# Optimization experiments

Measured on AMD Instinct MI355X. Metric: run time of the kernel, lower is better.

The kernel has to match this reference:

```python
import jax, jax.numpy as jnp
import numpy as np

N_G, N_D, D = 50000, 50000, 64
R, L, NNZ, B = 32, 2, 1600000, 2048
TEMP, LAMBDA_1, LAMBDA_2, DROPOUT = 0.2, 0.2, 1e-7, 0.1


def setup_inputs() -> dict:
    key = jax.random.key(0)
    ks = jax.random.split(key, 14)
    uids = jax.random.randint(ks[0], (B,), 0, N_G)
    iids = jax.random.randint(ks[1], (B,), 0, N_D)
    pos = jax.random.randint(ks[2], (B,), 0, N_D)
    neg = jax.random.randint(ks[3], (B,), 0, N_D)
    E_g_0 = jax.random.normal(ks[4], (N_G, D), jnp.float32) * 0.01
    E_d_0 = jax.random.normal(ks[5], (N_D, D), jnp.float32) * 0.01
    rows = jax.random.randint(ks[6], (NNZ,), 0, N_G)
    cols = jax.random.randint(ks[7], (NNZ,), 0, N_D)
    vals = jax.random.uniform(ks[8], (NNZ,), jnp.float32)
    g_mul_s = jax.random.normal(ks[9], (N_G, R), jnp.float32) * 0.1
    v_mul_s = jax.random.normal(ks[10], (N_D, R), jnp.float32) * 0.1
    ut = jax.random.normal(ks[11], (R, N_G), jnp.float32) * (N_G ** -0.5)
    vt = jax.random.normal(ks[12], (R, N_D), jnp.float32) * (N_D ** -0.5)
    drop_u = jax.random.uniform(ks[13], (L, 2, NNZ), jnp.float32)
    return {"uids": uids, "iids": iids, "pos": pos, "neg": neg,
            "E_g_0": E_g_0, "E_d_0": E_d_0, "rows": rows, "cols": cols,
            "vals": vals, "g_mul_s": g_mul_s, "v_mul_s": v_mul_s,
            "ut": ut, "vt": vt, "drop_u": drop_u}


def reference(uids, iids, pos, neg, E_g_0, E_d_0, rows, cols, vals,
              g_mul_s, v_mul_s, ut, vt, drop_u):
    # sparse_dropout keep masks (independent per layer and per spmm call)
    keep = (drop_u > DROPOUT).astype(vals.dtype) / (1.0 - DROPOUT)  # [L,2,NNZ]
    E_g, E_d = E_g_0, E_d_0
    E_g_sum, E_d_sum = E_g_0, E_d_0
    G_g_sum, G_d_sum = E_g_0, E_d_0
    for layer in range(L):
        # Z_g = dropout(A) @ E_d ; Z_d = dropout(A).T @ E_g  (COO spmm)
        vg = vals * keep[layer, 0]
        Z_g = jax.ops.segment_sum(vg[:, None] * E_d[cols], rows, num_segments=N_G)
        vd = vals * keep[layer, 1]
        Z_d = jax.ops.segment_sum(vd[:, None] * E_g[rows], cols, num_segments=N_D)
        # low-rank SVD branch
        G_g = g_mul_s @ (vt @ E_d)  # [n_g, d]
        G_d = v_mul_s @ (ut @ E_g)  # [n_d, d]
        E_g, E_d = Z_g, Z_d
        E_g_sum = E_g_sum + E_g
        E_d_sum = E_d_sum + E_d
        G_g_sum = G_g_sum + G_g
        G_d_sum = G_d_sum + G_d
    # InfoNCE-style contrastive loss (exactly as torch: log(sum exp + eps))
    S_g = (G_g_sum[uids] @ E_g_sum.T) / TEMP  # [B, n_g]
    S_d = (G_d_sum[iids] @ E_d_sum.T) / TEMP  # [B, n_d]
    neg_score = jnp.log(jnp.exp(S_g).sum(1) + 1e-8).mean() \
              + jnp.log(jnp.exp(S_d).sum(1) + 1e-8).mean()
    pos_score = jnp.clip((G_g_sum[uids] * E_g_sum[uids]).sum(1) / TEMP, -5.0, 5.0).mean() \
              + jnp.clip((G_d_sum[iids] * E_d_sum[iids]).sum(1) / TEMP, -5.0, 5.0).mean()
    loss_s = -pos_score + neg_score
    # BPR loss
    g_emb = E_g_sum[uids]
    diff = (g_emb * E_d_sum[pos]).sum(-1) - (g_emb * E_d_sum[neg]).sum(-1)
    loss_r = -jnp.log(jax.nn.sigmoid(diff)).mean()
    # L2 reg over trainable embedding params
    loss_reg = LAMBDA_2 * (jnp.sum(E_g_0 ** 2) + jnp.sum(E_d_0 ** 2))
    loss = loss_r + LAMBDA_1 * loss_s + loss_reg
    return (loss, loss_r, LAMBDA_1 * loss_s)
```

## Files before the change

kernel.cpp:

```cpp
#include <hip/hip_runtime.h>
#include <hip/hip_bf16.h>
#include <math.h>

#define N_Gc 50000
#define N_Dc 50000
#define DIM 64
#define RNK 32
#define NNZc 1600000
#define BSZ 2048
#define KEEPV (1.0f/0.9f)
#define INVT 5.0f
#define NBK2 196
#define NBLK 200
#define NSL 24
#define EPB 8000
#define MCH 256
#define MBLK 196

typedef __attribute__((ext_vector_type(8))) short bfrag;
typedef __attribute__((ext_vector_type(4))) float f32x4;

__device__ inline ushort f2bf(float f) {
  union { float f; unsigned int u; } v; v.f = f;
  unsigned int r = (v.u + 0x7fffu + ((v.u >> 16) & 1u)) >> 16;
  return (ushort)r;
}
__device__ inline float bf2f(ushort u) {
  union { unsigned int i; float f; } v; v.i = ((unsigned int)u) << 16;
  return v.f;
}

__global__ __launch_bounds__(256) void hist3_kernel(const int* __restrict__ rows, const int* __restrict__ cols,
                                                    int* __restrict__ cntR, int* __restrict__ cntC) {
  __shared__ int lh_r[NBK2];
  __shared__ int lh_c[NBK2];
  int t = threadIdx.x, blk = blockIdx.x;
  if (t < NBK2) { lh_r[t] = 0; lh_c[t] = 0; }
  __syncthreads();
  int e0 = blk*EPB;
  for (int i = e0 + t; i < e0 + EPB; i += 256) {
    atomicAdd(&lh_r[rows[i] >> 8], 1);
    atomicAdd(&lh_c[cols[i] >> 8], 1);
  }
  __syncthreads();
  if (t < NBK2) {
    cntR[t*NBLK + blk] = lh_r[t];
    cntC[t*NBLK + blk] = lh_c[t];
  }
}

__global__ __launch_bounds__(1024) void cscan2_kernel(const int* __restrict__ cntA, int* __restrict__ cbA, int* __restrict__ bpA,
                                                      const int* __restrict__ cntB, int* __restrict__ cbB, int* __restrict__ bpB) {
  const int n = NBK2*NBLK;
  const int* cnt = blockIdx.x ? cntB : cntA;
  int* cb = blockIdx.x ? cbB : cbA;
  int* bp = blockIdx.x ? bpB : bpA;
  __shared__ int wsum[16];
  int t = threadIdx.x, lane = t & 63, w = t >> 6;
  int carry = 0;
  for (int base = 0; base < n; base += 1024) {
    int i = base + t;
    int v = (i < n) ? cnt[i] : 0;
    int x = v;
    #pragma unroll
    for (int o = 1; o < 64; o <<= 1) { int y = __shfl_up(x, o); if (lane >= o) x += y; }
    if (lane == 63) wsum[w] = x;
    __syncthreads();
    if (t < 16) {
      int s = wsum[t];
      #pragma unroll
      for (int o = 1; o < 16; o <<= 1) { int y = __shfl_up(s, o); if (t >= o) s += y; }
      wsum[t] = s;
    }
    __syncthreads();
    int wpre = (w == 0) ? 0 : wsum[w-1];
    int total = wsum[15];
    int ex = carry + wpre + (x - v);
    if (i < n) {
      cb[i] = ex;
      if (i % NBLK == 0) bp[i/NBLK] = ex;
    }
    carry += total;
    __syncthreads();
  }
  if (t == 0) bp[NBK2] = carry;
}

__global__ __launch_bounds__(256) void phaseA2_kernel(const int* __restrict__ rows, const int* __restrict__ cols,
    const float* __restrict__ vals, const float* __restrict__ drop,
    const int* __restrict__ cbR, const int* __restrict__ cbC,
    uint2* __restrict__ stage_r, uint2* __restrict__ stage_c) {
  __shared__ int cnt_r[NBK2], cnt_c[NBK2];
  __shared__ int base_r[NBK2], base_c[NBK2];
  int t = threadIdx.x, blk = blockIdx.x;
  if (t < NBK2) {
    cnt_r[t] = 0; cnt_c[t] = 0;
    base_r[t] = cbR[t*NBLK + blk];
    base_c[t] = cbC[t*NBLK + blk];
  }
  __syncthreads();
  int e0 = blk*EPB;
  for (int i = e0 + t; i < e0 + EPB; i += 256) {
    int r = rows[i], c = cols[i];
    unsigned int vb = __float_as_uint(vals[i]);
    unsigned int dr0 = (drop[i] > 0.1f) ? (1u<<24) : 0u;
    unsigned int dc0 = (drop[(size_t)NNZc + i] > 0.1f) ? (1u<<24) : 0u;
    unsigned int dr1 = (drop[2*(size_t)NNZc + i] > 0.1f) ? (1u<<25) : 0u;
    unsigned int dc1 = (drop[3*(size_t)NNZc + i] > 0.1f) ? (1u<<25) : 0u;
    int br = r >> 8, bc = c >> 8;
    int p = base_r[br] + atomicAdd(&cnt_r[br], 1);
    stage_r[p] = make_uint2((unsigned int)c | ((unsigned int)(r & 255) << 16) | dr0 | dr1, vb);
    int q = base_c[bc] + atomicAdd(&cnt_c[bc], 1);
    stage_c[q] = make_uint2((unsigned int)r | ((unsigned int)(c & 255) << 16) | dc0 | dc1, vb);
  }
}

__global__ __launch_bounds__(256) void phaseB2_kernel(const int* __restrict__ bptr, int* __restrict__ ptrout,
    const uint2* __restrict__ stage, ushort* __restrict__ fcol,
    float* __restrict__ fw0, float* __restrict__ fw1, int n) {
  __shared__ int cnt[256];
  __shared__ int pos[256];
  __shared__ int woff[4];
  int t = threadIdx.x, b = blockIdx.x;
  int base_row = b*256;
  int base = bptr[b], endp = bptr[b+1];
  cnt[t] = 0;
  __syncthreads();
  for (int k = base + t; k < endp; k += 256)
    atomicAdd(&cnt[(stage[k].x >> 16) & 255], 1);
  __syncthreads();
  int lane = t & 63, w = t >> 6;
  int c = cnt[t], x = c;
  #pragma unroll
  for (int o = 1; o < 64; o <<= 1) { int y = __shfl_up(x, o); if (lane >= o) x += y; }
  if (lane == 63) woff[w] = x;
  __syncthreads();
  if (t == 0) { woff[1] += woff[0]; woff[2] += woff[1]; woff[3] += woff[2]; }
  __syncthreads();
  int excl = ((w == 0) ? 0 : woff[w-1]) + (x - c);
  pos[t] = excl;
  int rr = base_row + t;
  if (rr <= n) ptrout[rr] = base + excl;
  __syncthreads();
  for (int k = base + t; k < endp; k += 256) {
    uint2 rec = stage[k];
    int rel = (rec.x >> 16) & 255;
    int p = base + atomicAdd(&pos[rel], 1);
    float v = __uint_as_float(rec.y);
    fcol[p] = (ushort)(rec.x & 0xffffu);
    fw0[p] = (rec.x & (1u<<24)) ? v*KEEPV : 0.f;
    fw1[p] = (rec.x & (1u<<25)) ? v*KEEPV : 0.f;
  }
}

__global__ __launch_bounds__(256) void spmm_l0_kernel(const int* __restrict__ ptr,
    const ushort* __restrict__ fcol, const float* __restrict__ fw,
    const ushort* __restrict__ Eb, float* __restrict__ Z, ushort* __restrict__ Zb, int nrows) {
  int lane = threadIdx.x & 63;
  int row = blockIdx.x*4 + (threadIdx.x >> 6);
  if (row >= nrows) return;
  int k = ptr[row], end = ptr[row+1];
  float acc = 0.f;
  for (; k + 8 <= end; k += 8) {
    int cc[8]; float ww[8]; float gg[8];
    #pragma unroll
    for (int u = 0; u < 8; u++) { cc[u] = fcol[k+u]; ww[u] = fw[k+u]; }
    #pragma unroll
    for (int u = 0; u < 8; u++) gg[u] = bf2f(Eb[(size_t)cc[u]*DIM + lane]);
    #pragma unroll
    for (int u = 0; u < 8; u++) acc += ww[u]*gg[u];
  }
  for (; k < end; k++)
    acc += fw[k]*bf2f(Eb[(size_t)fcol[k]*DIM + lane]);
  size_t o = (size_t)row*DIM + lane;
  Z[o] = acc;
  Zb[o] = f2bf(acc);
}

__global__ __launch_bounds__(256) void spmm_l1_kernel(const int* __restrict__ ptr,
    const ushort* __restrict__ fcol, const float* __restrict__ fw,
    const ushort* __restrict__ Zb, const float* __restrict__ addA, const float* __restrict__ addB,
    ushort* __restrict__ Eout, int nrows) {
  int lane = threadIdx.x & 63;
  int row = blockIdx.x*4 + (threadIdx.x >> 6);
  if (row >= nrows) return;
  int k = ptr[row], end = ptr[row+1];
  float acc = 0.f;
  for (; k + 8 <= end; k += 8) {
    int cc[8]; float ww[8]; float gg[8];
    #pragma unroll
    for (int u = 0; u < 8; u++) { cc[u] = fcol[k+u]; ww[u] = fw[k+u]; }
    #pragma unroll
    for (int u = 0; u < 8; u++) gg[u] = bf2f(Zb[(size_t)cc[u]*DIM + lane]);
    #pragma unroll
    for (int u = 0; u < 8; u++) acc += ww[u]*gg[u];
  }
  for (; k < end; k++)
    acc += fw[k]*bf2f(Zb[(size_t)fcol[k]*DIM + lane]);
  size_t o = (size_t)row*DIM + lane;
  acc += addA[o] + addB[o];
  Eout[o] = f2bf(acc);
}

__global__ __launch_bounds__(256) void matred2_kernel(const float* __restrict__ vrow,
    const float* __restrict__ E0, const float* __restrict__ Z0,
    float* __restrict__ Mpart, int n) {
  __shared__ float vs[RNK*MCH];
  __shared__ float part[RNK*DIM];
  int t = threadIdx.x, lane = t & 63, w = t >> 6;
  int ci0 = blockIdx.x*MCH;
  int cnt = min(MCH, n - ci0);
  for (int idx = t; idx < RNK*DIM; idx += 256) part[idx] = 0.f;
  for (int idx = t; idx < RNK*MCH; idx += 256) {
    int r = idx >> 8, i = idx & (MCH-1);
    vs[idx] = (i < cnt) ? vrow[(size_t)r*n + ci0 + i] : 0.f;
  }
  __syncthreads();
  float acc[RNK];
  #pragma unroll
  for (int r = 0; r < RNK; r++) acc[r] = 0.f;
  int iw0 = w*64;
  for (int ii = 0; ii < 64; ii += 4) {
    int i = iw0 + ii;
    int gi = ci0 + i;
    float x0 = 0.f, x1 = 0.f, x2 = 0.f, x3 = 0.f;
    if (i + 3 < cnt) {
      x0 = E0[(size_t)(gi+0)*DIM + lane] + Z0[(size_t)(gi+0)*DIM + lane];
      x1 = E0[(size_t)(gi+1)*DIM + lane] + Z0[(size_t)(gi+1)*DIM + lane];
      x2 = E0[(size_t)(gi+2)*DIM + lane] + Z0[(size_t)(gi+2)*DIM + lane];
      x3 = E0[(size_t)(gi+3)*DIM + lane] + Z0[(size_t)(gi+3)*DIM + lane];
    } else {
      if (i+0 < cnt) x0 = E0[(size_t)(gi+0)*DIM + lane] + Z0[(size_t)(gi+0)*DIM + lane];
      if (i+1 < cnt) x1 = E0[(size_t)(gi+1)*DIM + lane] + Z0[(size_t)(gi+1)*DIM + lane];
      if (i+2 < cnt) x2 = E0[(size_t)(gi+2)*DIM + lane] + Z0[(size_t)(gi+2)*DIM + lane];
      if (i+3 < cnt) x3 = E0[(size_t)(gi+3)*DIM + lane] + Z0[(size_t)(gi+3)*DIM + lane];
    }
    #pragma unroll
    for (int r = 0; r < RNK; r++) {
      float4 v4 = *(const float4*)&vs[r*MCH + i];
      acc[r] += v4.x*x0 + v4.y*x1 + v4.z*x2 + v4.w*x3;
    }
  }
  #pragma unroll
  for (int r = 0; r < RNK; r++) atomicAdd(&part[r*DIM + lane], acc[r]);
  __syncthreads();
  float* dst = Mpart + (size_t)blockIdx.x*(RNK*DIM);
  for (int idx = t; idx < RNK*DIM; idx += 256) dst[idx] = part[idx];
}

__global__ __launch_bounds__(256) void mreduce_kernel(const float* __restrict__ Mpart,
    float* __restrict__ M, int nblk) {
  int idx = blockIdx.x*256 + threadIdx.x;
  if (idx < RNK*DIM) {
    float s = 0.f;
    for (int b = 0; b < nblk; b++) s += Mpart[(size_t)b*(RNK*DIM) + idx];
    M[idx] = s;
  }
}

__global__ __launch_bounds__(256) void gsmall_kernel(const int* __restrict__ ids,
    const float* __restrict__ E0, const float* __restrict__ mul, const float* __restrict__ M,
    float* __restrict__ out, ushort* __restrict__ outb) {
  __shared__ float Ms[RNK*DIM];
  int t = threadIdx.x;
  for (int i = t; i < RNK*DIM; i += 256) Ms[i] = M[i];
  __syncthreads();
  int b = blockIdx.x*4 + (t >> 6), lane = t & 63;
  int u = ids[b];
  float a = E0[(size_t)u*DIM + lane];
  #pragma unroll
  for (int r = 0; r < RNK; r++) a += mul[(size_t)u*RNK + r]*Ms[r*DIM + lane];
  out[(size_t)b*DIM + lane] = a;
  outb[(size_t)b*DIM + lane] = f2bf(a);
}

__global__ __launch_bounds__(256) void convsq_kernel(const float4* __restrict__ in,
    ushort4* __restrict__ out, int n4, float* __restrict__ acc) {
  __shared__ float ls[4];
  int t = threadIdx.x;
  int idx = blockIdx.x*256 + t;
  int stride = gridDim.x*256;
  float s = 0.f;
  for (int i = idx; i < n4; i += stride) {
    float4 v = in[i];
    ushort4 o;
    o.x = f2bf(v.x); o.y = f2bf(v.y); o.z = f2bf(v.z); o.w = f2bf(v.w);
    out[i] = o;
    s += v.x*v.x + v.y*v.y + v.z*v.z + v.w*v.w;
  }
  #pragma unroll
  for (int o = 32; o > 0; o >>= 1) s += __shfl_xor(s, o);
  if ((t & 63) == 0) ls[t >> 6] = s;
  __syncthreads();
  if (t == 0) atomicAdd(acc, ls[0] + ls[1] + ls[2] + ls[3]);
}

__global__ __launch_bounds__(256) void lse_mfma_kernel(const ushort* __restrict__ A,
    const ushort* __restrict__ X, int nj, float* __restrict__ sumexp) {
  __shared__ __align__(16) ushort Xs[64*68];
  int t = threadIdx.x, lane = t & 63, w = t >> 6;
  int bt = blockIdx.x & 31, js = blockIdx.x >> 5;
  int b0 = bt*64;
  int m = lane & 15, q = lane >> 4;
  const ushort* Arow = A + (size_t)(b0 + w*16 + m)*DIM + q*8;
  bfrag a0 = *(const bfrag*)(Arow);
  bfrag a1 = *(const bfrag*)(Arow + 32);
  float rs0 = 0.f, rs1 = 0.f, rs2 = 0.f, rs3 = 0.f;
  int njt = (nj + 63) >> 6;
  for (int jt = js; jt < njt; jt += NSL) {
    int j0 = jt << 6;
    __syncthreads();
    for (int c = t; c < 512; c += 256) {
      int r = c >> 3, k8 = (c & 7) << 3;
      int j = j0 + r;
      ushort4 v0 = {0,0,0,0}, v1 = {0,0,0,0};
      if (j < nj) {
        const ushort4* src = (const ushort4*)(X + (size_t)j*DIM + k8);
        v0 = src[0]; v1 = src[1];
      }
      *(ushort4*)&Xs[r*68 + k8]     = v0;
      *(ushort4*)&Xs[r*68 + k8 + 4] = v1;
    }
    __syncthreads();
    #pragma unroll
    for (int jq = 0; jq < 4; jq++) {
      int jr = jq*16 + m;
      union { bfrag f; uint2 u2[2]; } B0, B1;
      B0.u2[0] = *(const uint2*)&Xs[jr*68 + q*8];
      B0.u2[1] = *(const uint2*)&Xs[jr*68 + q*8 + 4];
      B1.u2[0] = *(const uint2*)&Xs[jr*68 + 32 + q*8];
      B1.u2[1] = *(const uint2*)&Xs[jr*68 + 32 + q*8 + 4];
      f32x4 acc = {0.f, 0.f, 0.f, 0.f};
      acc = __builtin_amdgcn_mfma_f32_16x16x32_bf16(a0, B0.f, acc, 0, 0, 0);
      acc = __builtin_amdgcn_mfma_f32_16x16x32_bf16(a1, B1.f, acc, 0, 0, 0);
      int jg = j0 + jr;
      if (jg < nj) {
        rs0 += __expf(acc[0]*INVT);
        rs1 += __expf(acc[1]*INVT);
        rs2 += __expf(acc[2]*INVT);
        rs3 += __expf(acc[3]*INVT);
      }
    }
  }
  #pragma unroll
  for (int o = 1; o < 16; o <<= 1) {
    rs0 += __shfl_xor(rs0, o);
    rs1 += __shfl_xor(rs1, o);
    rs2 += __shfl_xor(rs2, o);
    rs3 += __shfl_xor(rs3, o);
  }
  if (m == 0) {
    float* dst = &sumexp[b0 + w*16 + q*4];
    atomicAdd(&dst[0], rs0);
    atomicAdd(&dst[1], rs1);
    atomicAdd(&dst[2], rs2);
    atomicAdd(&dst[3], rs3);
  }
}

__global__ __launch_bounds__(256) void perb_kernel(const int* __restrict__ uids, const int* __restrict__ iids,
    const int* __restrict__ pos, const int* __restrict__ neg,
    const float* __restrict__ Ggu, const float* __restrict__ Gdi,
    const ushort* __restrict__ Egs_b, const ushort* __restrict__ Eds_b,
    const float* __restrict__ seg, const float* __restrict__ sed,
    float* __restrict__ accs) {
  __shared__ float lsum[3][4];
  int t = threadIdx.x, lane = t & 63, w = t >> 6;
  int b = blockIdx.x*4 + w;
  int u = uids[b], it = iids[b], p = pos[b], ng = neg[b];
  float egu = bf2f(Egs_b[(size_t)u*DIM + lane]);
  float d1 = Ggu[(size_t)b*DIM + lane]*egu;
  float d2 = Gdi[(size_t)b*DIM + lane]*bf2f(Eds_b[(size_t)it*DIM + lane]);
  float d3 = egu*bf2f(Eds_b[(size_t)p*DIM + lane]);
  float d4 = egu*bf2f(Eds_b[(size_t)ng*DIM + lane]);
  #pragma unroll
  for (int o = 32; o > 0; o >>= 1) {
    d1 += __shfl_xor(d1, o);
    d2 += __shfl_xor(d2, o);
    d3 += __shfl_xor(d3, o);
    d4 += __shfl_xor(d4, o);
  }
  if (lane == 0) {
    float pterm = fminf(fmaxf(d1*INVT, -5.f), 5.f) + fminf(fmaxf(d2*INVT, -5.f), 5.f);
    float diff = d3 - d4;
    lsum[0][w] = pterm;
    lsum[1][w] = log1pf(expf(-diff));
    lsum[2][w] = logf(seg[b] + 1e-8f) + logf(sed[b] + 1e-8f);
  }
  __syncthreads();
  if (t < 3) atomicAdd(&accs[t], lsum[t][0] + lsum[t][1] + lsum[t][2] + lsum[t][3]);
}

__global__ void final_kernel(const float* __restrict__ accs, float* __restrict__ out) {
  float posm = accs[0]*(1.f/BSZ);
  float lr   = accs[1]*(1.f/BSZ);
  float negm = accs[2]*(1.f/BSZ);
  float reg  = 1e-7f*accs[3];
  float l1ls = 0.2f*(negm - posm);
  out[0] = lr + l1ls + reg;
  out[1] = lr;
  out[2] = l1ls;
}

extern "C" void kernel_launch(void* const* d_in, const int* in_sizes, int n_in,
                              void* d_out, int out_size, void* d_ws, size_t ws_size,
                              hipStream_t stream) {
  (void)in_sizes; (void)n_in; (void)out_size;
  const int*   uids = (const int*)d_in[0];
  const int*   iids = (const int*)d_in[1];
  const int*   pos  = (const int*)d_in[2];
  const int*   neg  = (const int*)d_in[3];
  const float* Eg0  = (const float*)d_in[4];
  const float* Ed0  = (const float*)d_in[5];
  const int*   rows = (const int*)d_in[6];
  const int*   cols = (const int*)d_in[7];
  const float* vals = (const float*)d_in[8];
  const float* gms  = (const float*)d_in[9];
  const float* vms  = (const float*)d_in[10];
  const float* ut   = (const float*)d_in[11];
  const float* vt   = (const float*)d_in[12];
  const float* drop = (const float*)d_in[13];
  float* out = (float*)d_out;

  float* ws = (float*)d_ws;
  const size_t ED = (size_t)N_Gc*DIM;
  float* Zg0  = ws;
  float* Zd0  = Zg0 + ED;
  float* REG1 = Zd0 + ED;
  float* REG2 = REG1 + ED;
  int* ptr_r = (int*)(REG2 + ED);
  int* ptr_c = ptr_r + (N_Gc + 1);
  int* bptr_r = ptr_c + (N_Dc + 1);
  int* bptr_c = bptr_r + (NBK2 + 1);
  int* cntR = bptr_c + (NBK2 + 1);
  int* cntC = cntR + NBK2*NBLK;
  int* cbR  = cntC + NBK2*NBLK;
  int* cbC  = cbR + NBK2*NBLK;
  ushort* fcol_r = (ushort*)(cbC + NBK2*NBLK);
  float* fw_r0  = (float*)(fcol_r + NNZc);
  float* fw_r1  = fw_r0 + NNZc;
  ushort* fcol_c = (ushort*)(fw_r1 + NNZc);
  float* fw_c0  = (float*)(fcol_c + NNZc);
  float* fw_c1  = fw_c0 + NNZc;
  float* Ggu = fw_c1 + NNZc;
  float* Gdi = Ggu + (size_t)BSZ*DIM;
  ushort* Ggu_b = (ushort*)(Gdi + (size_t)BSZ*DIM);
  ushort* Gdi_b = Ggu_b + (size_t)BSZ*DIM;
  float* Mg  = (float*)(Gdi_b + (size_t)BSZ*DIM);
  float* Md  = Mg + RNK*DIM;
  float* seg = Md + RNK*DIM;
  float* sed = seg + BSZ;
  float* accs = sed + BSZ;
  float* MpG = accs + 16;
  float* MpD = MpG + (size_t)MBLK*RNK*DIM;

  uint2* stage_r = (uint2*)Zg0;
  uint2* stage_c = (uint2*)REG1;
  ushort* Eg0_b = (ushort*)REG1;
  ushort* Ed0_b = Eg0_b + ED;
  ushort* Egs_b = (ushort*)REG1;
  ushort* Eds_b = Egs_b + ED;
  ushort* Zg0_b = (ushort*)REG2;
  ushort* Zd0_b = Zg0_b + ED;

  size_t need = ((char*)(MpD + (size_t)MBLK*RNK*DIM)) - ((char*)d_ws);
  if (ws_size < need) return;

  hipMemsetAsync(seg, 0, sizeof(float)*(2*BSZ + 16), stream);

  hist3_kernel<<<NBLK, 256, 0, stream>>>(rows, cols, cntR, cntC);
  cscan2_kernel<<<2, 1024, 0, stream>>>(cntR, cbR, bptr_r, cntC, cbC, bptr_c);
  phaseA2_kernel<<<NBLK, 256, 0, stream>>>(rows, cols, vals, drop, cbR, cbC, stage_r, stage_c);
  phaseB2_kernel<<<NBK2, 256, 0, stream>>>(bptr_r, ptr_r, stage_r, fcol_r, fw_r0, fw_r1, N_Gc);
  phaseB2_kernel<<<NBK2, 256, 0, stream>>>(bptr_c, ptr_c, stage_c, fcol_c, fw_c0, fw_c1, N_Dc);

  int n4 = (int)(ED/4);
  convsq_kernel<<<1024, 256, 0, stream>>>((const float4*)Eg0, (ushort4*)Eg0_b, n4, accs + 3);
  convsq_kernel<<<1024, 256, 0, stream>>>((const float4*)Ed0, (ushort4*)Ed0_b, n4, accs + 3);

  int spmm_blocks = (N_Gc + 3)/4;
  spmm_l0_kernel<<<spmm_blocks, 256, 0, stream>>>(ptr_r, fcol_r, fw_r0, Ed0_b, Zg0, Zg0_b, N_Gc);
  spmm_l0_kernel<<<spmm_blocks, 256, 0, stream>>>(ptr_c, fcol_c, fw_c0, Eg0_b, Zd0, Zd0_b, N_Dc);
  spmm_l1_kernel<<<spmm_blocks, 256, 0, stream>>>(ptr_r, fcol_r, fw_r1, Zd0_b, Eg0, Zg0, Egs_b, N_Gc);
  spmm_l1_kernel<<<spmm_blocks, 256, 0, stream>>>(ptr_c, fcol_c, fw_c1, Zg0_b, Ed0, Zd0, Eds_b, N_Dc);

  matred2_kernel<<<MBLK, 256, 0, stream>>>(vt, Ed0, Zd0, MpG, N_Dc);
  matred2_kernel<<<MBLK, 256, 0, stream>>>(ut, Eg0, Zg0, MpD, N_Gc);
  mreduce_kernel<<<(RNK*DIM + 255)/256, 256, 0, stream>>>(MpG, Mg, MBLK);
  mreduce_kernel<<<(RNK*DIM + 255)/256, 256, 0, stream>>>(MpD, Md, MBLK);

  gsmall_kernel<<<BSZ/4, 256, 0, stream>>>(uids, Eg0, gms, Mg, Ggu, Ggu_b);
  gsmall_kernel<<<BSZ/4, 256, 0, stream>>>(iids, Ed0, vms, Md, Gdi, Gdi_b);

  lse_mfma_kernel<<<32*NSL, 256, 0, stream>>>(Ggu_b, Egs_b, N_Gc, seg);
  lse_mfma_kernel<<<32*NSL, 256, 0, stream>>>(Gdi_b, Eds_b, N_Dc, sed);

  perb_kernel<<<BSZ/4, 256, 0, stream>>>(uids, iids, pos, neg, Ggu, Gdi, Egs_b, Eds_b, seg, sed, accs);
  final_kernel<<<1, 1, 0, stream>>>(accs, out);
}
```

Baseline: 687.2 us.

## Merge paired kernels via blockIdx.y, drop fp32 Z buffers, add nontemporal loads and prefetch

Each pair of row-side and column-side kernel launches (phaseB2, convsq, spmm l0/l1, matred2, mreduce, gsmall, lse) becomes a single launch with a second grid dimension choosing the side. Launch count drops and the two independent halves can run concurrently. The fp32 Z intermediates are removed: later stages read the bf16 copies, which cuts workspace and traffic but adds bf16 rounding to the residual sums. Streaming data now uses nontemporal loads and stores, the spmm index/weight fetch is software-prefetched one chunk ahead, and the LSE slice count is doubled.

```diff
diff --git a/kernel.cpp b/kernel.cpp
--- a/kernel.cpp
+++ b/kernel.cpp
@@ -12,13 +12,14 @@
 #define INVT 5.0f
 #define NBK2 196
 #define NBLK 200
-#define NSL 24
+#define NSL 48
 #define EPB 8000
 #define MCH 256
 #define MBLK 196
 
 typedef __attribute__((ext_vector_type(8))) short bfrag;
 typedef __attribute__((ext_vector_type(4))) float f32x4;
+typedef unsigned long long u64;
 
 __device__ inline ushort f2bf(float f) {
   union { float f; unsigned int u; } v; v.f = f;
@@ -39,8 +40,8 @@
   __syncthreads();
   int e0 = blk*EPB;
   for (int i = e0 + t; i < e0 + EPB; i += 256) {
-    atomicAdd(&lh_r[rows[i] >> 8], 1);
-    atomicAdd(&lh_c[cols[i] >> 8], 1);
+    atomicAdd(&lh_r[__builtin_nontemporal_load(&rows[i]) >> 8], 1);
+    atomicAdd(&lh_c[__builtin_nontemporal_load(&cols[i]) >> 8], 1);
   }
   __syncthreads();
   if (t < NBK2) {
@@ -89,7 +90,7 @@
 __global__ __launch_bounds__(256) void phaseA2_kernel(const int* __restrict__ rows, const int* __restrict__ cols,
     const float* __restrict__ vals, const float* __restrict__ drop,
     const int* __restrict__ cbR, const int* __restrict__ cbC,
-    uint2* __restrict__ stage_r, uint2* __restrict__ stage_c) {
+    u64* __restrict__ stage_r, u64* __restrict__ stage_c) {
   __shared__ int cnt_r[NBK2], cnt_c[NBK2];
   __shared__ int base_r[NBK2], base_c[NBK2];
   int t = threadIdx.x, blk = blockIdx.x;
@@ -101,23 +102,35 @@
   __syncthreads();
   int e0 = blk*EPB;
   for (int i = e0 + t; i < e0 + EPB; i += 256) {
-    int r = rows[i], c = cols[i];
-    unsigned int vb = __float_as_uint(vals[i]);
-    unsigned int dr0 = (drop[i] > 0.1f) ? (1u<<24) : 0u;
-    unsigned int dc0 = (drop[(size_t)NNZc + i] > 0.1f) ? (1u<<24) : 0u;
-    unsigned int dr1 = (drop[2*(size_t)NNZc + i] > 0.1f) ? (1u<<25) : 0u;
-    unsigned int dc1 = (drop[3*(size_t)NNZc + i] > 0.1f) ? (1u<<25) : 0u;
+    int r = __builtin_nontemporal_load(&rows[i]);
+    int c = __builtin_nontemporal_load(&cols[i]);
+    u64 vb = (u64)__float_as_uint(__builtin_nontemporal_load(&vals[i])) << 32;
+    unsigned int dr0 = (__builtin_nontemporal_load(&drop[i]) > 0.1f) ? (1u<<24) : 0u;
+    unsigned int dc0 = (__builtin_nontemporal_load(&drop[(size_t)NNZc + i]) > 0.1f) ? (1u<<24) : 0u;
+    unsigned int dr1 = (__builtin_nontemporal_load(&drop[2*(size_t)NNZc + i]) > 0.1f) ? (1u<<25) : 0u;
+    unsigned int dc1 = (__builtin_nontemporal_load(&drop[3*(size_t)NNZc + i]) > 0.1f) ? (1u<<25) : 0u;
     int br = r >> 8, bc = c >> 8;
     int p = base_r[br] + atomicAdd(&cnt_r[br], 1);
-    stage_r[p] = make_uint2((unsigned int)c | ((unsigned int)(r & 255) << 16) | dr0 | dr1, vb);
+    u64 recr = vb | (unsigned int)c | ((unsigned int)(r & 255) << 16) | dr0 | dr1;
+    __builtin_nontemporal_store(recr, &stage_r[p]);
     int q = base_c[bc] + atomicAdd(&cnt_c[bc], 1);
-    stage_c[q] = make_uint2((unsigned int)r | ((unsigned int)(c & 255) << 16) | dc0 | dc1, vb);
-  }
-}
-
-__global__ __launch_bounds__(256) void phaseB2_kernel(const int* __restrict__ bptr, int* __restrict__ ptrout,
-    const uint2* __restrict__ stage, ushort* __restrict__ fcol,
-    float* __restrict__ fw0, float* __restrict__ fw1, int n) {
+    u64 recc = vb | (unsigned int)r | ((unsigned int)(c & 255) << 16) | dc0 | dc1;
+    __builtin_nontemporal_store(recc, &stage_c[q]);
+  }
+}
+
+__global__ __launch_bounds__(256) void phaseB2_kernel(
+    const int* __restrict__ bptrR, int* __restrict__ ptroutR, const u64* __restrict__ stageR,
+    ushort* __restrict__ fcolR, float* __restrict__ fw0R, float* __restrict__ fw1R,
+    const int* __restrict__ bptrC, int* __restrict__ ptroutC, const u64* __restrict__ stageC,
+    ushort* __restrict__ fcolC, float* __restrict__ fw0C, float* __restrict__ fw1C, int n) {
+  const int side = blockIdx.y;
+  const int* bptr = side ? bptrC : bptrR;
+  int* ptrout = side ? ptroutC : ptroutR;
+  const u64* stage = side ? stageC : stageR;
+  ushort* fcol = side ? fcolC : fcolR;
+  float* fw0 = side ? fw0C : fw0R;
+  float* fw1 = side ? fw1C : fw1R;
   __shared__ int cnt[256];
   __shared__ int pos[256];
   __shared__ int woff[4];
@@ -126,8 +139,10 @@
   int base = bptr[b], endp = bptr[b+1];
   cnt[t] = 0;
   __syncthreads();
-  for (int k = base + t; k < endp; k += 256)
-    atomicAdd(&cnt[(stage[k].x >> 16) & 255], 1);
+  for (int k = base + t; k < endp; k += 256) {
+    unsigned int lo = (unsigned int)__builtin_nontemporal_load(&stage[k]);
+    atomicAdd(&cnt[(lo >> 16) & 255], 1);
+  }
   __syncthreads();
   int lane = t & 63, w = t >> 6;
   int c = cnt[t], x = c;
@@ -143,68 +158,100 @@
   if (rr <= n) ptrout[rr] = base + excl;
   __syncthreads();
   for (int k = base + t; k < endp; k += 256) {
-    uint2 rec = stage[k];
-    int rel = (rec.x >> 16) & 255;
+    u64 rec = __builtin_nontemporal_load(&stage[k]);
+    unsigned int lo = (unsigned int)rec;
+    int rel = (lo >> 16) & 255;
     int p = base + atomicAdd(&pos[rel], 1);
-    float v = __uint_as_float(rec.y);
-    fcol[p] = (ushort)(rec.x & 0xffffu);
-    fw0[p] = (rec.x & (1u<<24)) ? v*KEEPV : 0.f;
-    fw1[p] = (rec.x & (1u<<25)) ? v*KEEPV : 0.f;
-  }
-}
-
-__global__ __launch_bounds__(256) void spmm_l0_kernel(const int* __restrict__ ptr,
-    const ushort* __restrict__ fcol, const float* __restrict__ fw,
-    const ushort* __restrict__ Eb, float* __restrict__ Z, ushort* __restrict__ Zb, int nrows) {
+    float v = __uint_as_float((unsigned int)(rec >> 32));
+    __builtin_nontemporal_store((ushort)(lo & 0xffffu), &fcol[p]);
+    __builtin_nontemporal_store((lo & (1u<<24)) ? v*KEEPV : 0.f, &fw0[p]);
+    __builtin_nontemporal_store((lo & (1u<<25)) ? v*KEEPV : 0.f, &fw1[p]);
+  }
+}
+
+__device__ __forceinline__ float spmm_row(const ushort* __restrict__ fcol, const float* __restrict__ fw,
+                                          const ushort* __restrict__ Eb, int k0, int end, int lane) {
+  float acc = 0.f;
+  int nfull = (end - k0) >> 3;
+  int cc[8]; float ww[8];
+  if (nfull > 0) {
+    #pragma unroll
+    for (int u = 0; u < 8; u++) {
+      cc[u] = __builtin_nontemporal_load(&fcol[k0+u]);
+      ww[u] = __builtin_nontemporal_load(&fw[k0+u]);
+    }
+    for (int b = 1; b < nfull; b++) {
+      int kn = k0 + b*8;
+      int cn[8]; float wn[8];
+      #pragma unroll
+      for (int u = 0; u < 8; u++) {
+        cn[u] = __builtin_nontemporal_load(&fcol[kn+u]);
+        wn[u] = __builtin_nontemporal_load(&fw[kn+u]);
+      }
+      #pragma unroll
+      for (int u = 0; u < 8; u++) acc += ww[u]*bf2f(Eb[(size_t)cc[u]*DIM + lane]);
+      #pragma unroll
+      for (int u = 0; u < 8; u++) { cc[u] = cn[u]; ww[u] = wn[u]; }
+    }
+    #pragma unroll
+    for (int u = 0; u < 8; u++) acc += ww[u]*bf2f(Eb[(size_t)cc[u]*DIM + lane]);
+  }
+  for (int k = k0 + nfull*8; k < end; k++)
+    acc += __builtin_nontemporal_load(&fw[k])*bf2f(Eb[(size_t)__builtin_nontemporal_load(&fcol[k])*DIM + lane]);
+  return acc;
+}
+
+__global__ __launch_bounds__(256) void spmm_l0_kernel(
+    const int* __restrict__ ptrR, const ushort* __restrict__ fcolR, const float* __restrict__ fwR,
+    const ushort* __restrict__ EbR, ushort* __restrict__ ZbR,
+    const int* __restrict__ ptrC, const ushort* __restrict__ fcolC, const float* __restrict__ fwC,
+    const ushort* __restrict__ EbC, ushort* __restrict__ ZbC, int nrows) {
+  const int side = blockIdx.y;
+  const int* ptr = side ? ptrC : ptrR;
+  const ushort* fcol = side ? fcolC : fcolR;
+  const float* fw = side ? fwC : fwR;
+  const ushort* Eb = side ? EbC : EbR;
+  ushort* Zb = side ? ZbC : ZbR;
   int lane = threadIdx.x & 63;
   int row = blockIdx.x*4 + (threadIdx.x >> 6);
   if (row >= nrows) return;
-  int k = ptr[row], end = ptr[row+1];
-  float acc = 0.f;
-  for (; k + 8 <= end; k += 8) {
-    int cc[8]; float ww[8]; float gg[8];
-    #pragma unroll
-    for (int u = 0; u < 8; u++) { cc[u] = fcol[k+u]; ww[u] = fw[k+u]; }
-    #pragma unroll
-    for (int u = 0; u < 8; u++) gg[u] = bf2f(Eb[(size_t)cc[u]*DIM + lane]);
-    #pragma unroll
-    for (int u = 0; u < 8; u++) acc += ww[u]*gg[u];
-  }
-  for (; k < end; k++)
-    acc += fw[k]*bf2f(Eb[(size_t)fcol[k]*DIM + lane]);
-  size_t o = (size_t)row*DIM + lane;
-  Z[o] = acc;
-  Zb[o] = f2bf(acc);
-}
-
-__global__ __launch_bounds__(256) void spmm_l1_kernel(const int* __restrict__ ptr,
-    const ushort* __restrict__ fcol, const float* __restrict__ fw,
-    const ushort* __restrict__ Zb, const float* __restrict__ addA, const float* __restrict__ addB,
-    ushort* __restrict__ Eout, int nrows) {
+  float acc = spmm_row(fcol, fw, Eb, ptr[row], ptr[row+1], lane);
+  Zb[(size_t)row*DIM + lane] = f2bf(acc);
+}
+
+__global__ __launch_bounds__(256) void spmm_l1_kernel(
+    const int* __restrict__ ptrR, const ushort* __restrict__ fcolR, const float* __restrict__ fwR,
+    const ushort* __restrict__ ZbOR, const float* __restrict__ E0R, const ushort* __restrict__ ZbSR,
+    ushort* __restrict__ EoutR,
+    const int* __restrict__ ptrC, const ushort* __restrict__ fcolC, const float* __restrict__ fwC,
+    const ushort* __restrict__ ZbOC, const float* __restrict__ E0C, const ushort* __restrict__ ZbSC,
+    ushort* __restrict__ EoutC, int nrows) {
+  const int side = blockIdx.y;
+  const int* ptr = side ? ptrC : ptrR;
+  const ushort* fcol = side ? fcolC : fcolR;
+  const float* fw = side ? fwC : fwR;
+  const ushort* ZbO = side ? ZbOC : ZbOR;
+  const float* E0 = side ? E0C : E0R;
+  const ushort* ZbS = side ? ZbSC : ZbSR;
+  ushort* Eout = side ? EoutC : EoutR;
   int lane = threadIdx.x & 63;
   int row = blockIdx.x*4 + (threadIdx.x >> 6);
   if (row >= nrows) return;
-  int k = ptr[row], end = ptr[row+1];
-  float acc = 0.f;
-  for (; k + 8 <= end; k += 8) {
-    int cc[8]; float ww[8]; float gg[8];
-    #pragma unroll
-    for (int u = 0; u < 8; u++) { cc[u] = fcol[k+u]; ww[u] = fw[k+u]; }
-    #pragma unroll
-    for (int u = 0; u < 8; u++) gg[u] = bf2f(Zb[(size_t)cc[u]*DIM + lane]);
-    #pragma unroll
-    for (int u = 0; u < 8; u++) acc += ww[u]*gg[u];
-  }
-  for (; k < end; k++)
-    acc += fw[k]*bf2f(Zb[(size_t)fcol[k]*DIM + lane]);
+  float acc = spmm_row(fcol, fw, ZbO, ptr[row], ptr[row+1], lane);
   size_t o = (size_t)row*DIM + lane;
-  acc += addA[o] + addB[o];
+  acc += __builtin_nontemporal_load(&E0[o]) + bf2f(ZbS[o]);
   Eout[o] = f2bf(acc);
 }
 
-__global__ __launch_bounds__(256) void matred2_kernel(const float* __restrict__ vrow,
-    const float* __restrict__ E0, const float* __restrict__ Z0,
-    float* __restrict__ Mpart, int n) {
+__global__ __launch_bounds__(256) void matred2_kernel(
+    const float* __restrict__ vrowA, const float* __restrict__ E0A, const ushort* __restrict__ ZbA, float* __restrict__ MpA,
+    const float* __restrict__ vrowB, const float* __restrict__ E0B, const ushort* __restrict__ ZbB, float* __restrict__ MpB,
+    int n) {
+  const int side = blockIdx.y;
+  const float* vrow = side ? vrowB : vrowA;
+  const float* E0 = side ? E0B : E0A;
+  const ushort* Zb = side ? ZbB : ZbA;
+  float* Mpart = side ? MpB : MpA;
   __shared__ float vs[RNK*MCH];
   __shared__ float part[RNK*DIM];
   int t = threadIdx.x, lane = t & 63, w = t >> 6;
@@ -213,7 +260,7 @@
   for (int idx = t; idx < RNK*DIM; idx += 256) part[idx] = 0.f;
   for (int idx = t; idx < RNK*MCH; idx += 256) {
     int r = idx >> 8, i = idx & (MCH-1);
-    vs[idx] = (i < cnt) ? vrow[(size_t)r*n + ci0 + i] : 0.f;
+    vs[idx] = (i < cnt) ? __builtin_nontemporal_load(&vrow[(size_t)r*n + ci0 + i]) : 0.f;
   }
   __syncthreads();
   float acc[RNK];
@@ -224,17 +271,10 @@
     int i = iw0 + ii;
     int gi = ci0 + i;
     float x0 = 0.f, x1 = 0.f, x2 = 0.f, x3 = 0.f;
-    if (i + 3 < cnt) {
-      x0 = E0[(size_t)(gi+0)*DIM + lane] + Z0[(size_t)(gi+0)*DIM + lane];
-      x1 = E0[(size_t)(gi+1)*DIM + lane] + Z0[(size_t)(gi+1)*DIM + lane];
-      x2 = E0[(size_t)(gi+2)*DIM + lane] + Z0[(size_t)(gi+2)*DIM + lane];
-      x3 = E0[(size_t)(gi+3)*DIM + lane] + Z0[(size_t)(gi+3)*DIM + lane];
-    } else {
-      if (i+0 < cnt) x0 = E0[(size_t)(gi+0)*DIM + lane] + Z0[(size_t)(gi+0)*DIM + lane];
-      if (i+1 < cnt) x1 = E0[(size_t)(gi+1)*DIM + lane] + Z0[(size_t)(gi+1)*DIM + lane];
-      if (i+2 < cnt) x2 = E0[(size_t)(gi+2)*DIM + lane] + Z0[(size_t)(gi+2)*DIM + lane];
-      if (i+3 < cnt) x3 = E0[(size_t)(gi+3)*DIM + lane] + Z0[(size_t)(gi+3)*DIM + lane];
-    }
+    if (i+0 < cnt) x0 = E0[(size_t)(gi+0)*DIM + lane] + bf2f(Zb[(size_t)(gi+0)*DIM + lane]);
+    if (i+1 < cnt) x1 = E0[(size_t)(gi+1)*DIM + lane] + bf2f(Zb[(size_t)(gi+1)*DIM + lane]);
+    if (i+2 < cnt) x2 = E0[(size_t)(gi+2)*DIM + lane] + bf2f(Zb[(size_t)(gi+2)*DIM + lane]);
+    if (i+3 < cnt) x3 = E0[(size_t)(gi+3)*DIM + lane] + bf2f(Zb[(size_t)(gi+3)*DIM + lane]);
     #pragma unroll
     for (int r = 0; r < RNK; r++) {
       float4 v4 = *(const float4*)&vs[r*MCH + i];
@@ -248,8 +288,10 @@
   for (int idx = t; idx < RNK*DIM; idx += 256) dst[idx] = part[idx];
 }
 
-__global__ __launch_bounds__(256) void mreduce_kernel(const float* __restrict__ Mpart,
-    float* __restrict__ M, int nblk) {
+__global__ __launch_bounds__(256) void mreduce_kernel(const float* __restrict__ MpA, float* __restrict__ MA,
+                                                      const float* __restrict__ MpB, float* __restrict__ MB, int nblk) {
+  const float* Mpart = blockIdx.y ? MpB : MpA;
+  float* M = blockIdx.y ? MB : MA;
   int idx = blockIdx.x*256 + threadIdx.x;
   if (idx < RNK*DIM) {
     float s = 0.f;
@@ -258,9 +300,18 @@
   }
 }
 
-__global__ __launch_bounds__(256) void gsmall_kernel(const int* __restrict__ ids,
-    const float* __restrict__ E0, const float* __restrict__ mul, const float* __restrict__ M,
-    float* __restrict__ out, ushort* __restrict__ outb) {
+__global__ __launch_bounds__(256) void gsmall_kernel(
+    const int* __restrict__ idsA, const float* __restrict__ E0A, const float* __restrict__ mulA,
+    const float* __restrict__ MA, float* __restrict__ outA, ushort* __restrict__ outbA,
+    const int* __restrict__ idsB, const float* __restrict__ E0B, const float* __restrict__ mulB,
+    const float* __restrict__ MB, float* __restrict__ outB, ushort* __restrict__ outbB) {
+  const int side = blockIdx.y;
+  const int* ids = side ? idsB : idsA;
+  const float* E0 = side ? E0B : E0A;
+  const float* mul = side ? mulB : mulA;
+  const float* M = side ? MB : MA;
+  float* out = side ? outB : outA;
+  ushort* outb = side ? outbB : outbA;
   __shared__ float Ms[RNK*DIM];
   int t = threadIdx.x;
   for (int i = t; i < RNK*DIM; i += 256) Ms[i] = M[i];
@@ -274,18 +325,21 @@
   outb[(size_t)b*DIM + lane] = f2bf(a);
 }
 
-__global__ __launch_bounds__(256) void convsq_kernel(const float4* __restrict__ in,
-    ushort4* __restrict__ out, int n4, float* __restrict__ acc) {
+__global__ __launch_bounds__(256) void convsq_kernel(const float* __restrict__ inA, ushort* __restrict__ outA,
+                                                     const float* __restrict__ inB, ushort* __restrict__ outB,
+                                                     int n4, float* __restrict__ acc) {
+  const float* in = blockIdx.y ? inB : inA;
+  ushort* out = blockIdx.y ? outB : outA;
   __shared__ float ls[4];
   int t = threadIdx.x;
   int idx = blockIdx.x*256 + t;
   int stride = gridDim.x*256;
   float s = 0.f;
   for (int i = idx; i < n4; i += stride) {
-    float4 v = in[i];
+    float4 v = *(const float4*)&in[(size_t)i*4];
     ushort4 o;
     o.x = f2bf(v.x); o.y = f2bf(v.y); o.z = f2bf(v.z); o.w = f2bf(v.w);
-    out[i] = o;
+    *(ushort4*)&out[(size_t)i*4] = o;
     s += v.x*v.x + v.y*v.y + v.z*v.z + v.w*v.w;
   }
   #pragma unroll
@@ -295,8 +349,13 @@
   if (t == 0) atomicAdd(acc, ls[0] + ls[1] + ls[2] + ls[3]);
 }
 
-__global__ __launch_bounds__(256) void lse_mfma_kernel(const ushort* __restrict__ A,
-    const ushort* __restrict__ X, int nj, float* __restrict__ sumexp) {
+__global__ __launch_bounds__(256) void lse_mfma_kernel(
+    const ushort* __restrict__ Ag, const ushort* __restrict__ Xg, float* __restrict__ seg,
+    const ushort* __restrict__ Ad, const ushort* __restrict__ Xd, float* __restrict__ sed,
+    int nj) {
+  const ushort* A = blockIdx.y ? Ad : Ag;
+  const ushort* X = blockIdx.y ? Xd : Xg;
+  float* sumexp = blockIdx.y ? sed : seg;
   __shared__ __align__(16) ushort Xs[64*68];
   int t = threadIdx.x, lane = t & 63, w = t >> 6;
   int bt = blockIdx.x & 31, js = blockIdx.x >> 5;
@@ -424,11 +483,9 @@
 
   float* ws = (float*)d_ws;
   const size_t ED = (size_t)N_Gc*DIM;
-  float* Zg0  = ws;
-  float* Zd0  = Zg0 + ED;
-  float* REG1 = Zd0 + ED;
-  float* REG2 = REG1 + ED;
-  int* ptr_r = (int*)(REG2 + ED);
+  float* REG_A = ws;
+  float* REG_B = REG_A + ED;
+  int* ptr_r = (int*)(REG_B + ED);
   int* ptr_c = ptr_r + (N_Gc + 1);
   int* bptr_r = ptr_c + (N_Dc + 1);
   int* bptr_c = bptr_r + (NBK2 + 1);
@@ -454,14 +511,14 @@
   float* MpG = accs + 16;
   float* MpD = MpG + (size_t)MBLK*RNK*DIM;
 
-  uint2* stage_r = (uint2*)Zg0;
-  uint2* stage_c = (uint2*)REG1;
-  ushort* Eg0_b = (ushort*)REG1;
+  u64* stage_r = (u64*)REG_A;
+  u64* stage_c = (u64*)REG_B;
+  ushort* Zg0_b = (ushort*)REG_A;
+  ushort* Zd0_b = Zg0_b + ED;
+  ushort* Eg0_b = (ushort*)REG_B;
   ushort* Ed0_b = Eg0_b + ED;
-  ushort* Egs_b = (ushort*)REG1;
+  ushort* Egs_b = (ushort*)REG_B;
   ushort* Eds_b = Egs_b + ED;
-  ushort* Zg0_b = (ushort*)REG2;
-  ushort* Zd0_b = Zg0_b + ED;
 
   size_t need = ((char*)(MpD + (size_t)MBLK*RNK*DIM)) - ((char*)d_ws);
   if (ws_size < need) return;
@@ -471,29 +528,31 @@
   hist3_kernel<<<NBLK, 256, 0, stream>>>(rows, cols, cntR, cntC);
   cscan2_kernel<<<2, 1024, 0, stream>>>(cntR, cbR, bptr_r, cntC, cbC, bptr_c);
   phaseA2_kernel<<<NBLK, 256, 0, stream>>>(rows, cols, vals, drop, cbR, cbC, stage_r, stage_c);
-  phaseB2_kernel<<<NBK2, 256, 0, stream>>>(bptr_r, ptr_r, stage_r, fcol_r, fw_r0, fw_r1, N_Gc);
-  phaseB2_kernel<<<NBK2, 256, 0, stream>>>(bptr_c, ptr_c, stage_c, fcol_c, fw_c0, fw_c1, N_Dc);
+  phaseB2_kernel<<<dim3(NBK2, 2), 256, 0, stream>>>(
+      bptr_r, ptr_r, stage_r, fcol_r, fw_r0, fw_r1,
+      bptr_c, ptr_c, stage_c, fcol_c, fw_c0, fw_c1, N_Gc);
 
   int n4 = (int)(ED/4);
-  convsq_kernel<<<1024, 256, 0, stream>>>((const float4*)Eg0, (ushort4*)Eg0_b, n4, accs + 3);
-  convsq_kernel<<<1024, 256, 0, stream>>>((const float4*)Ed0, (ushort4*)Ed0_b, n4, accs + 3);
+  convsq_kernel<<<dim3(1024, 2), 256, 0, stream>>>(Eg0, Eg0_b, Ed0, Ed0_b, n4, accs + 3);
 
   int spmm_blocks = (N_Gc + 3)/4;
-  spmm_l0_kernel<<<spmm_blocks, 256, 0, stream>>>(ptr_r, fcol_r, fw_r0, Ed0_b, Zg0, Zg0_b, N_Gc);
-  spmm_l0_kernel<<<spmm_blocks, 256, 0, stream>>>(ptr_c, fcol_c, fw_c0, Eg0_b, Zd0, Zd0_b, N_Dc);
-  spmm_l1_kernel<<<spmm_blocks, 256, 0, stream>>>(ptr_r, fcol_r, fw_r1, Zd0_b, Eg0, Zg0, Egs_b, N_Gc);
-  spmm_l1_kernel<<<spmm_blocks, 256, 0, stream>>>(ptr_c, fcol_c, fw_c1, Zg0_b, Ed0, Zd0, Eds_b, N_Dc);
-
-  matred2_kernel<<<MBLK, 256, 0, stream>>>(vt, Ed0, Zd0, MpG, N_Dc);
-  matred2_kernel<<<MBLK, 256, 0, stream>>>(ut, Eg0, Zg0, MpD, N_Gc);
-  mreduce_kernel<<<(RNK*DIM + 255)/256, 256, 0, stream>>>(MpG, Mg, MBLK);
-  mreduce_kernel<<<(RNK*DIM + 255)/256, 256, 0, stream>>>(MpD, Md, MBLK);
-
-  gsmall_kernel<<<BSZ/4, 256, 0, stream>>>(uids, Eg0, gms, Mg, Ggu, Ggu_b);
-  gsmall_kernel<<<BSZ/4, 256, 0, stream>>>(iids, Ed0, vms, Md, Gdi, Gdi_b);
-
-  lse_mfma_kernel<<<32*NSL, 256, 0, stream>>>(Ggu_b, Egs_b, N_Gc, seg);
-  lse_mfma_kernel<<<32*NSL, 256, 0, stream>>>(Gdi_b, Eds_b, N_Dc, sed);
+  spmm_l0_kernel<<<dim3(spmm_blocks, 2), 256, 0, stream>>>(
+      ptr_r, fcol_r, fw_r0, Ed0_b, Zg0_b,
+      ptr_c, fcol_c, fw_c0, Eg0_b, Zd0_b, N_Gc);
+  spmm_l1_kernel<<<dim3(spmm_blocks, 2), 256, 0, stream>>>(
+      ptr_r, fcol_r, fw_r1, Zd0_b, Eg0, Zg0_b, Egs_b,
+      ptr_c, fcol_c, fw_c1, Zg0_b, Ed0, Zd0_b, Eds_b, N_Gc);
+
+  matred2_kernel<<<dim3(MBLK, 2), 256, 0, stream>>>(
+      vt, Ed0, Zd0_b, MpG,
+      ut, Eg0, Zg0_b, MpD, N_Dc);
+  mreduce_kernel<<<dim3((RNK*DIM + 255)/256, 2), 256, 0, stream>>>(MpG, Mg, MpD, Md, MBLK);
+
+  gsmall_kernel<<<dim3(BSZ/4, 2), 256, 0, stream>>>(
+      uids, Eg0, gms, Mg, Ggu, Ggu_b,
+      iids, Ed0, vms, Md, Gdi, Gdi_b);
+
+  lse_mfma_kernel<<<dim3(32*NSL, 2), 256, 0, stream>>>(Ggu_b, Egs_b, seg, Gdi_b, Eds_b, sed, N_Gc);
 
   perb_kernel<<<BSZ/4, 256, 0, stream>>>(uids, iids, pos, neg, Ggu, Gdi, Egs_b, Eds_b, seg, sed, accs);
   final_kernel<<<1, 1, 0, stream>>>(accs, out);
```

Measured after the change: 961.9 us. 1.4x slower.
